# Performance work log

Measured on AMD Instinct MI355X. Metric: run time of the kernel, lower is better.

Reference implementation:

```python
import jax, jax.numpy as jnp
import numpy as np

N, E, D = 10000, 160000, 256
EPS = 1e-5


def layer_norm(x, gamma, beta):
    mu = jnp.mean(x, axis=-1, keepdims=True)
    var = jnp.var(x, axis=-1, keepdims=True)
    return (x - mu) * jax.lax.rsqrt(var + EPS) * gamma + beta


def mlp(x, w1, b1, w2, b2):
    return jax.nn.relu(x @ w1 + b1) @ w2 + b2


def setup_inputs() -> dict:
    key = jax.random.key(0)
    ks = jax.random.split(key, 16)
    s = lambda fan_in: 1.0 / np.sqrt(fan_in)
    inp = {
        'x': jax.random.normal(ks[0], (N, D), jnp.float32),
        'edge_index': jax.random.randint(ks[1], (2, E), 0, N, jnp.int64),
        'edge_attr': jax.random.normal(ks[2], (E, D), jnp.float32),
        # edge MLP: in 3D=768 -> hidden 2D=512 -> out D=256, then LN
        'e_w1': jax.random.uniform(ks[3], (3 * D, 2 * D), jnp.float32, -s(3 * D), s(3 * D)),
        'e_b1': jnp.zeros((2 * D,), jnp.float32),
        'e_w2': jax.random.uniform(ks[4], (2 * D, D), jnp.float32, -s(2 * D), s(2 * D)),
        'e_b2': jnp.zeros((D,), jnp.float32),
        'e_g': jnp.ones((D,), jnp.float32),
        'e_beta': jnp.zeros((D,), jnp.float32),
        # node MLP: in 2D=512 -> hidden 2D=512 -> out D=256, then LN
        'n_w1': jax.random.uniform(ks[5], (2 * D, 2 * D), jnp.float32, -s(2 * D), s(2 * D)),
        'n_b1': jnp.zeros((2 * D,), jnp.float32),
        'n_w2': jax.random.uniform(ks[6], (2 * D, D), jnp.float32, -s(2 * D), s(2 * D)),
        'n_b2': jnp.zeros((D,), jnp.float32),
        'n_g': jnp.ones((D,), jnp.float32),
        'n_beta': jnp.zeros((D,), jnp.float32),
    }
    return inp


def reference(x, edge_index, edge_attr, e_w1, e_b1, e_w2, e_b2, e_g, e_beta,
              n_w1, n_b1, n_w2, n_b2, n_g, n_beta):
    i, j = edge_index[0], edge_index[1]
    # Edge processor: gather, concat, MLP + LN, residual
    h = jnp.concatenate([x[i], x[j], edge_attr], axis=-1)  # [E, 3D]
    new_edge = edge_attr + layer_norm(mlp(h, e_w1, e_b1, e_w2, e_b2), e_g, e_beta)
    # Node processor: scatter-add over j, concat, MLP + LN, residual
    agg = jax.ops.segment_sum(new_edge, j, num_segments=x.shape[0])  # [N, D]
    hn = jnp.concatenate([x, agg], axis=-1)  # [N, 2D]
    new_x = x + layer_norm(mlp(hn, n_w1, n_b1, n_w2, n_b2), n_g, n_beta)
    return new_x, new_edge
```

## Files before the change

kernel.cpp:

```cpp
#include <hip/hip_runtime.h>

#define NNODE 10000
#define NEDGE 160000
#define DD 256

using f32x4  = __attribute__((ext_vector_type(4))) float;
using bf16x8 = __attribute__((ext_vector_type(8))) short;
using u32x4  = __attribute__((ext_vector_type(4))) unsigned;

__device__ inline short f2bf(float f) {
  unsigned u = __float_as_uint(f);
  unsigned r = (u + 0x7fffu + ((u >> 16) & 1u)) >> 16;
  return (short)(unsigned short)r;
}

__device__ inline float bf2f(short s) {
  return __uint_as_float(((unsigned)(unsigned short)s) << 16);
}

__device__ inline unsigned pkbf(float a, float b) {
  unsigned r;
  asm("v_cvt_pk_bf16_f32 %0, %1, %2" : "=v"(r) : "v"(a), "v"(b));
  return r;
}

__global__ void cast_x_kernel(const float* __restrict__ x, short* __restrict__ xb, int total) {
  int i = blockIdx.x * 256 + threadIdx.x;
  if (i < total) xb[i] = f2bf(x[i]);
}

__global__ void pack_w_kernel(const float* __restrict__ w, short* __restrict__ p, int K, int N) {
  int idx = blockIdx.x * 256 + threadIdx.x;
  if (idx >= K * N) return;
  int k = idx / N, n = idx - k * N;
  p[(size_t)(k >> 3) * N * 8 + (size_t)n * 8 + (k & 7)] = f2bf(w[idx]);
}

__global__ void pack_ew1_kernel(const float* __restrict__ w, short* __restrict__ w1ap,
                                short* __restrict__ w1bp, short* __restrict__ w1cp) {
  int idx = blockIdx.x * 256 + threadIdx.x;
  if (idx >= 768 * 512) return;
  int k = idx >> 9, n = idx & 511;
  short v = f2bf(w[idx]);
  int kk = k & 255;
  short* dst = (k < 256) ? w1ap : (k < 512) ? w1bp : w1cp;
  dst[(size_t)(kk >> 3) * 512 * 8 + (size_t)n * 8 + (kk & 7)] = v;
}

__global__ void hist_kernel(const int* __restrict__ ei, int* __restrict__ deg) {
  int e = blockIdx.x * 256 + threadIdx.x;
  if (e < NEDGE) {
    int j = ei[NEDGE + e]; j = min(max(j, 0), NNODE - 1);
    atomicAdd(&deg[j], 1);
  }
}

__global__ void scan_kernel(const int* __restrict__ deg, int* __restrict__ row_start) {
  __shared__ int part[256];
  int t = threadIdx.x;
  const int CH = 40;
  int base = t * CH;
  int s = 0;
  for (int i = 0; i < CH; i++) {
    int idx = base + i;
    s += (idx < NNODE) ? deg[idx] : 0;
  }
  part[t] = s;
  __syncthreads();
  for (int off = 1; off < 256; off <<= 1) {
    int v = (t >= off) ? part[t - off] : 0;
    __syncthreads();
    part[t] += v;
    __syncthreads();
  }
  int run = (t == 0) ? 0 : part[t - 1];
  for (int i = 0; i < CH; i++) {
    int idx = base + i;
    if (idx < NNODE) { row_start[idx] = run; run += deg[idx]; }
  }
  if (t == 255) row_start[NNODE] = part[255];
}

__global__ void scatter_kernel(const int* __restrict__ ei, const int* __restrict__ row_start,
                               int* __restrict__ cursor, int* __restrict__ csr) {
  int e = blockIdx.x * 256 + threadIdx.x;
  if (e < NEDGE) {
    int j = ei[NEDGE + e]; j = min(max(j, 0), NNODE - 1);
    int p = atomicAdd(&cursor[j], 1);
    csr[row_start[j] + p] = e;
  }
}

__global__ __launch_bounds__(256, 2)
void precomp_pab(const short* __restrict__ xb, const short* __restrict__ w1bp,
                 short* __restrict__ pab) {
  __shared__ __align__(16) short abuf[2048 * 8];

  const int tid  = threadIdx.x;
  const int lane = tid & 63;
  const int wid  = tid >> 6;
  const int lhi  = lane >> 4;
  const int llo  = lane & 15;
  const int swz  = llo & 7;
  const int m0   = blockIdx.x * 64;

  #pragma unroll
  for (int q = 0; q < 8; q++) {
    int S = wid * 512 + q * 64 + lane;
    int row = S >> 5;
    int segp = S & 31;
    int seg = segp ^ (row & 7);
    int rowg = min(m0 + row, NNODE - 1);
    __builtin_amdgcn_global_load_lds(
        (const int*)((const char*)xb + (size_t)rowg * 512 + seg * 16),
        (int*)(abuf + (size_t)(wid * 512 + q * 64) * 8), 16, 0, 0);
  }
  __syncthreads();

  f32x4 acc1[4][8] = {};
  const bf16x8* bp1 = (const bf16x8*)w1bp;
  #pragma unroll
  for (int kk = 0; kk < 256; kk += 32) {
    const int ks = kk >> 3;
    bf16x8 a[4];
    #pragma unroll
    for (int mf = 0; mf < 4; mf++)
      a[mf] = *(const bf16x8*)(abuf + ((mf * 16 + llo) * 32 + ((ks + lhi) ^ swz)) * 8);
    const bf16x8* bb = bp1 + (size_t)(ks + lhi) * 512 + wid * 128 + llo;
    #pragma unroll
    for (int nf = 0; nf < 8; nf++) {
      bf16x8 b = bb[nf * 16];
      #pragma unroll
      for (int mf = 0; mf < 4; mf++)
        acc1[mf][nf] = __builtin_amdgcn_mfma_f32_16x16x32_bf16(a[mf], b, acc1[mf][nf], 0, 0, 0);
    }
  }

  #pragma unroll
  for (int mf = 0; mf < 4; mf++) {
    #pragma unroll
    for (int r = 0; r < 4; r++) {
      int row = m0 + mf * 16 + lhi * 4 + r;
      if (row < NNODE) {
        u32x4 wv = { pkbf(acc1[mf][0][r], acc1[mf][1][r]),
                     pkbf(acc1[mf][2][r], acc1[mf][3][r]),
                     pkbf(acc1[mf][4][r], acc1[mf][5][r]),
                     pkbf(acc1[mf][6][r], acc1[mf][7][r]) };
        *(u32x4*)(pab + (size_t)row * 512 + llo * 32 + wid * 8) = wv;
      }
    }
  }
}

__global__ __launch_bounds__(256, 2)
void fused_edge(const int* __restrict__ ei,
                const int* __restrict__ csr,
                const float* __restrict__ ea,
                const short* __restrict__ xb,
                const short* __restrict__ pab,
                const short* __restrict__ w1ap,
                const short* __restrict__ w1cp,
                const float* __restrict__ b1,
                const short* __restrict__ w2p,
                const float* __restrict__ b2,
                const float* __restrict__ gam,
                const float* __restrict__ bet,
                float* __restrict__ out,
                float* __restrict__ aggf)
{
  __shared__ __align__(16) char smem[66560];
  __shared__ int eidx[64], idxi[64], idxj[64];
  __shared__ float pS[256], pQ[256];

  short* abufE = (short*)smem;
  short* hid   = (short*)smem;
  float* outt  = (float*)smem;

  const int tid  = threadIdx.x;
  const int lane = tid & 63;
  const int wid  = tid >> 6;
  const int lhi  = lane >> 4;
  const int llo  = lane & 15;
  const int swz  = llo & 7;
  const int m0   = blockIdx.x * 64;
  const int bcol2 = wid * 64 + llo;

  if (tid < 64) {
    int e = csr[m0 + tid];
    eidx[tid] = e;
    int a = ei[e];
    int b = ei[NEDGE + e];
    idxi[tid] = min(max(a, 0), NNODE - 1);
    idxj[tid] = min(max(b, 0), NNODE - 1);
  }
  __syncthreads();

  const short* pXi[4];
  #pragma unroll
  for (int mf = 0; mf < 4; mf++)
    pXi[mf] = xb + (size_t)idxi[mf * 16 + llo] * DD;

  #pragma unroll
  for (int q = 0; q < 8; q++) {
    int S = q * 256 + tid;
    int row = S >> 5;
    int segp = S & 31;
    int seg = segp ^ (row & 7);
    const f32x4* src = (const f32x4*)(ea + (size_t)eidx[row] * 256 + seg * 8);
    f32x4 u0 = __builtin_nontemporal_load(src);
    f32x4 u1 = __builtin_nontemporal_load(src + 1);
    u32x4 qv = { pkbf(u0.x, u0.y), pkbf(u0.z, u0.w), pkbf(u1.x, u1.y), pkbf(u1.z, u1.w) };
    *(u32x4*)(abufE + (size_t)S * 8) = qv;
  }
  __syncthreads();

  f32x4 acc1[4][8] = {};
  {
    const bf16x8* bpC = (const bf16x8*)w1cp;
    #pragma unroll
    for (int kk = 0; kk < 256; kk += 32) {
      const int ks = kk >> 3;
      bf16x8 a[4];
      #pragma unroll
      for (int mf = 0; mf < 4; mf++)
        a[mf] = *(const bf16x8*)(abufE + ((mf * 16 + llo) * 32 + ((ks + lhi) ^ swz)) * 8);
      const bf16x8* bb = bpC + (size_t)(ks + lhi) * 512 + wid * 128 + llo;
      #pragma unroll
      for (int nf = 0; nf < 8; nf++) {
        bf16x8 b = bb[nf * 16];
        #pragma unroll
        for (int mf = 0; mf < 4; mf++)
          acc1[mf][nf] = __builtin_amdgcn_mfma_f32_16x16x32_bf16(a[mf], b, acc1[mf][nf], 0, 0, 0);
      }
    }
    const bf16x8* bpA = (const bf16x8*)w1ap;
    #pragma unroll
    for (int kk = 0; kk < 256; kk += 32) {
      const int ks = kk >> 3;
      bf16x8 a[4];
      #pragma unroll
      for (int mf = 0; mf < 4; mf++)
        a[mf] = *(const bf16x8*)(pXi[mf] + kk + lhi * 8);
      const bf16x8* bb = bpA + (size_t)(ks + lhi) * 512 + wid * 128 + llo;
      #pragma unroll
      for (int nf = 0; nf < 8; nf++) {
        bf16x8 b = bb[nf * 16];
        #pragma unroll
        for (int mf = 0; mf < 4; mf++)
          acc1[mf][nf] = __builtin_amdgcn_mfma_f32_16x16x32_bf16(a[mf], b, acc1[mf][nf], 0, 0, 0);
      }
    }
  }

  #pragma unroll
  for (int mf = 0; mf < 4; mf++) {
    #pragma unroll
    for (int r = 0; r < 4; r++) {
      int row = mf * 16 + lhi * 4 + r;
      int gj = idxj[row];
      bf16x8 pb = *(const bf16x8*)(pab + (size_t)gj * 512 + llo * 32 + wid * 8);
      #pragma unroll
      for (int nf = 0; nf < 8; nf++)
        acc1[mf][nf][r] += bf2f(pb[nf]);
    }
  }

  float resv[4][4][4];
  #pragma unroll
  for (int mf = 0; mf < 4; mf++) {
    #pragma unroll
    for (int r = 0; r < 4; r++) {
      int row = mf * 16 + lhi * 4 + r;
      #pragma unroll
      for (int nf = 0; nf < 4; nf++) {
        int col = bcol2 + nf * 16;
        resv[mf][r][nf] = bf2f(abufE[row * 256 + (((col >> 3) ^ (row & 7)) << 3) + (col & 7)]);
      }
    }
  }
  __syncthreads();

  #pragma unroll
  for (int nf = 0; nf < 8; nf++) {
    int col = wid * 128 + nf * 16 + llo;
    float bb = b1[col];
    int cs = col >> 3, cl = col & 7;
    #pragma unroll
    for (int mf = 0; mf < 4; mf++) {
      #pragma unroll
      for (int r = 0; r < 4; r++) {
        int row = mf * 16 + lhi * 4 + r;
        float v = acc1[mf][nf][r] + bb;
        v = v > 0.f ? v : 0.f;
        hid[row * 512 + ((cs ^ (row & 7)) * 8) + cl] = f2bf(v);
      }
    }
  }
  __syncthreads();

  f32x4 acc2[4][4] = {};
  const bf16x8* bp2 = (const bf16x8*)w2p;
  #pragma unroll
  for (int kk = 0; kk < 512; kk += 32) {
    const int ks = kk >> 3;
    bf16x8 a[4];
    #pragma unroll
    for (int mf = 0; mf < 4; mf++) {
      int row = mf * 16 + llo;
      a[mf] = *(const bf16x8*)(hid + row * 512 + (((ks + lhi) ^ swz) * 8));
    }
    const bf16x8* bb = bp2 + (size_t)(ks + lhi) * 256 + bcol2;
    #pragma unroll
    for (int nf = 0; nf < 4; nf++) {
      bf16x8 b = bb[nf * 16];
      #pragma unroll
      for (int mf = 0; mf < 4; mf++)
        acc2[mf][nf] = __builtin_amdgcn_mfma_f32_16x16x32_bf16(a[mf], b, acc2[mf][nf], 0, 0, 0);
    }
  }

  float bb2[4], gg[4], be[4];
  #pragma unroll
  for (int nf = 0; nf < 4; nf++) {
    int col = bcol2 + nf * 16;
    bb2[nf] = b2[col]; gg[nf] = gam[col]; be[nf] = bet[col];
  }
  #pragma unroll
  for (int mf = 0; mf < 4; mf++)
    #pragma unroll
    for (int nf = 0; nf < 4; nf++)
      #pragma unroll
      for (int r = 0; r < 4; r++)
        acc2[mf][nf][r] += bb2[nf];

  float S[4][4], Q[4][4];
  #pragma unroll
  for (int mf = 0; mf < 4; mf++) {
    #pragma unroll
    for (int r = 0; r < 4; r++) {
      float s = 0.f, q = 0.f;
      #pragma unroll
      for (int nf = 0; nf < 4; nf++) {
        float v = acc2[mf][nf][r];
        s += v; q += v * v;
      }
      S[mf][r] = s; Q[mf][r] = q;
    }
  }
  #pragma unroll
  for (int m = 1; m <= 8; m <<= 1) {
    #pragma unroll
    for (int mf = 0; mf < 4; mf++)
      #pragma unroll
      for (int r = 0; r < 4; r++) {
        S[mf][r] += __shfl_xor(S[mf][r], m);
        Q[mf][r] += __shfl_xor(Q[mf][r], m);
      }
  }
  if (llo == 0) {
    #pragma unroll
    for (int mf = 0; mf < 4; mf++)
      #pragma unroll
      for (int r = 0; r < 4; r++) {
        int row = mf * 16 + lhi * 4 + r;
        pS[wid * 64 + row] = S[mf][r];
        pQ[wid * 64 + row] = Q[mf][r];
      }
  }
  __syncthreads();

  float mu[4][4], rsv[4][4];
  #pragma unroll
  for (int mf = 0; mf < 4; mf++) {
    #pragma unroll
    for (int r = 0; r < 4; r++) {
      int row = mf * 16 + lhi * 4 + r;
      float s = pS[row] + pS[64 + row] + pS[128 + row] + pS[192 + row];
      float q = pQ[row] + pQ[64 + row] + pQ[128 + row] + pQ[192 + row];
      float m_ = s * (1.f / 256.f);
      mu[mf][r]  = m_;
      rsv[mf][r] = rsqrtf(q * (1.f / 256.f) - m_ * m_ + 1e-5f);
    }
  }

  #pragma unroll
  for (int mf = 0; mf < 4; mf++) {
    #pragma unroll
    for (int r = 0; r < 4; r++) {
      int row = mf * 16 + lhi * 4 + r;
      #pragma unroll
      for (int nf = 0; nf < 4; nf++) {
        float v = (acc2[mf][nf][r] - mu[mf][r]) * rsv[mf][r] * gg[nf] + be[nf]
                  + resv[mf][r][nf];
        outt[row * 260 + bcol2 + nf * 16] = v;
      }
    }
  }
  __syncthreads();

  #pragma unroll
  for (int it = 0; it < 16; it++) {
    int row = it * 4 + wid;
    int e = eidx[row];
    f32x4 o4 = *((const f32x4*)(outt + row * 260) + lane);
    __builtin_nontemporal_store(o4, (f32x4*)(out + (size_t)e * 256) + lane);
  }
  __syncthreads();

  {
    int c = tid;
    float acc = 0.f;
    int cj = idxj[0];
    #pragma unroll 8
    for (int r = 0; r < 64; r++) {
      int jr = idxj[r];
      if (jr != cj) {
        atomicAdd(&aggf[(size_t)cj * 256 + c], acc);
        acc = 0.f; cj = jr;
      }
      acc += outt[r * 260 + c];
    }
    atomicAdd(&aggf[(size_t)cj * 256 + c], acc);
  }
}

__global__ __launch_bounds__(256, 2)
void fused_node(const float* __restrict__ x,
                const short* __restrict__ xb,
                const float* __restrict__ aggf,
                const short* __restrict__ w1p,
                const float* __restrict__ b1,
                const short* __restrict__ w2p,
                const float* __restrict__ b2,
                const float* __restrict__ gam,
                const float* __restrict__ bet,
                float* __restrict__ out)
{
  constexpr int HP = 520;
  __shared__ __align__(16) short hid[64 * HP];
  __shared__ float pS[4][64], pQ[4][64];

  const int tid  = threadIdx.x;
  const int lane = tid & 63;
  const int wid  = tid >> 6;
  const int m0   = blockIdx.x * 64;
  const int lhi  = lane >> 4;
  const int llo  = lane & 15;

  const short* pI[4]; const float* pJ[4];
  #pragma unroll
  for (int mf = 0; mf < 4; mf++) {
    int rr = min(m0 + mf * 16 + llo, NNODE - 1);
    pI[mf] = xb + (size_t)rr * DD;
    pJ[mf] = aggf + (size_t)rr * DD;
  }

  f32x4 acc1[4][8] = {};
  const bf16x8* bp1 = (const bf16x8*)w1p;
  const int bcol1 = wid * 128 + llo;

  #pragma unroll
  for (int s = 0; s < 8; s++) {
    #pragma unroll
    for (int kk = 0; kk < 64; kk += 32) {
      const int ko = s * 64 + kk + lhi * 8;
      bf16x8 a[4];
      #pragma unroll
      for (int mf = 0; mf < 4; mf++) {
        if (s < 4) {
          a[mf] = *(const bf16x8*)(pI[mf] + ko);
        } else {
          const float* fp = pJ[mf] + (ko - 256);
          f32x4 u0 = *(const f32x4*)fp;
          f32x4 u1 = *(const f32x4*)(fp + 4);
          u32x4 q = { pkbf(u0.x, u0.y), pkbf(u0.z, u0.w),
                      pkbf(u1.x, u1.y), pkbf(u1.z, u1.w) };
          a[mf] = __builtin_bit_cast(bf16x8, q);
        }
      }
      const bf16x8* bb = bp1 + (size_t)(s * 8 + (kk >> 3) + lhi) * 512 + bcol1;
      #pragma unroll
      for (int nf = 0; nf < 8; nf++) {
        bf16x8 b = bb[nf * 16];
        #pragma unroll
        for (int mf = 0; mf < 4; mf++)
          acc1[mf][nf] = __builtin_amdgcn_mfma_f32_16x16x32_bf16(a[mf], b, acc1[mf][nf], 0, 0, 0);
      }
    }
  }

  #pragma unroll
  for (int nf = 0; nf < 8; nf++) {
    int col = wid * 128 + nf * 16 + llo;
    float bb = b1[col];
    #pragma unroll
    for (int mf = 0; mf < 4; mf++) {
      #pragma unroll
      for (int r = 0; r < 4; r++) {
        float v = acc1[mf][nf][r] + bb;
        v = v > 0.f ? v : 0.f;
        hid[(mf * 16 + lhi * 4 + r) * HP + col] = f2bf(v);
      }
    }
  }
  __syncthreads();

  f32x4 acc2[4][4] = {};
  const bf16x8* bp2 = (const bf16x8*)w2p;
  const int bcol2 = wid * 64 + llo;
  #pragma unroll
  for (int kk = 0; kk < 512; kk += 32) {
    bf16x8 a[4];
    #pragma unroll
    for (int mf = 0; mf < 4; mf++)
      a[mf] = *(const bf16x8*)(hid + (mf * 16 + llo) * HP + kk + lhi * 8);
    const bf16x8* bb = bp2 + (size_t)((kk >> 3) + lhi) * 256 + bcol2;
    #pragma unroll
    for (int nf = 0; nf < 4; nf++) {
      bf16x8 b = bb[nf * 16];
      #pragma unroll
      for (int mf = 0; mf < 4; mf++)
        acc2[mf][nf] = __builtin_amdgcn_mfma_f32_16x16x32_bf16(a[mf], b, acc2[mf][nf], 0, 0, 0);
    }
  }

  float bb2[4], gg[4], be[4];
  #pragma unroll
  for (int nf = 0; nf < 4; nf++) {
    int col = bcol2 + nf * 16;
    bb2[nf] = b2[col]; gg[nf] = gam[col]; be[nf] = bet[col];
  }
  #pragma unroll
  for (int mf = 0; mf < 4; mf++)
    #pragma unroll
    for (int nf = 0; nf < 4; nf++)
      #pragma unroll
      for (int r = 0; r < 4; r++)
        acc2[mf][nf][r] += bb2[nf];

  float S[4][4], Q[4][4];
  #pragma unroll
  for (int mf = 0; mf < 4; mf++) {
    #pragma unroll
    for (int r = 0; r < 4; r++) {
      float s = 0.f, q = 0.f;
      #pragma unroll
      for (int nf = 0; nf < 4; nf++) {
        float v = acc2[mf][nf][r];
        s += v; q += v * v;
      }
      S[mf][r] = s; Q[mf][r] = q;
    }
  }
  #pragma unroll
  for (int m = 1; m <= 8; m <<= 1) {
    #pragma unroll
    for (int mf = 0; mf < 4; mf++)
      #pragma unroll
      for (int r = 0; r < 4; r++) {
        S[mf][r] += __shfl_xor(S[mf][r], m);
        Q[mf][r] += __shfl_xor(Q[mf][r], m);
      }
  }
  if (llo == 0) {
    #pragma unroll
    for (int mf = 0; mf < 4; mf++)
      #pragma unroll
      for (int r = 0; r < 4; r++) {
        int row = mf * 16 + lhi * 4 + r;
        pS[wid][row] = S[mf][r];
        pQ[wid][row] = Q[mf][r];
      }
  }
  __syncthreads();

  float mu[4][4], rsv[4][4];
  #pragma unroll
  for (int mf = 0; mf < 4; mf++) {
    #pragma unroll
    for (int r = 0; r < 4; r++) {
      int row = mf * 16 + lhi * 4 + r;
      float s = pS[0][row] + pS[1][row] + pS[2][row] + pS[3][row];
      float q = pQ[0][row] + pQ[1][row] + pQ[2][row] + pQ[3][row];
      float m_ = s * (1.f / 256.f);
      mu[mf][r]  = m_;
      rsv[mf][r] = rsqrtf(q * (1.f / 256.f) - m_ * m_ + 1e-5f);
    }
  }

  #pragma unroll
  for (int mf = 0; mf < 4; mf++) {
    #pragma unroll
    for (int r = 0; r < 4; r++) {
      int grow = m0 + mf * 16 + lhi * 4 + r;
      if (grow >= NNODE) continue;
      const float* rp = x   + (size_t)grow * DD + bcol2;
      float*       op = out + (size_t)grow * DD + bcol2;
      #pragma unroll
      for (int nf = 0; nf < 4; nf++) {
        float v = (acc2[mf][nf][r] - mu[mf][r]) * rsv[mf][r] * gg[nf] + be[nf] + rp[nf * 16];
        op[nf * 16] = v;
      }
    }
  }
}

extern "C" void kernel_launch(void* const* d_in, const int* in_sizes, int n_in,
                              void* d_out, int out_size, void* d_ws, size_t ws_size,
                              hipStream_t stream) {
  const float* x      = (const float*)d_in[0];
  const int*   ei     = (const int*)  d_in[1];
  const float* ea     = (const float*)d_in[2];
  const float* e_w1   = (const float*)d_in[3];
  const float* e_b1   = (const float*)d_in[4];
  const float* e_w2   = (const float*)d_in[5];
  const float* e_b2   = (const float*)d_in[6];
  const float* e_g    = (const float*)d_in[7];
  const float* e_beta = (const float*)d_in[8];
  const float* n_w1   = (const float*)d_in[9];
  const float* n_b1   = (const float*)d_in[10];
  const float* n_w2   = (const float*)d_in[11];
  const float* n_b2   = (const float*)d_in[12];
  const float* n_g    = (const float*)d_in[13];
  const float* n_beta = (const float*)d_in[14];

  float* out_x = (float*)d_out;
  float* out_e = (float*)d_out + (size_t)NNODE * DD;

  char* w = (char*)d_ws;
  short* xb    = (short*)(w);
  short* pab   = (short*)(w + 5120000);
  short* w1ap  = (short*)(w + 15360000);
  short* w1bp  = (short*)(w + 15622144);
  short* w1cp  = (short*)(w + 15884288);
  short* ew2p  = (short*)(w + 16146432);
  short* nw1p  = (short*)(w + 16408576);
  short* nw2p  = (short*)(w + 16932864);
  float* aggf  = (float*)(w + 17195008);
  int*   deg   = (int*)  (w + 27435008);
  int*   cur   = (int*)  (w + 27475968);
  int*   rs    = (int*)  (w + 27516928);
  int*   csr   = (int*)  (w + 27557904);

  hipMemsetAsync(deg, 0, 81920, stream);
  hipMemsetAsync(aggf, 0, (size_t)NNODE * DD * sizeof(float), stream);

  cast_x_kernel<<<(NNODE * DD + 255) / 256, 256, 0, stream>>>(x, xb, NNODE * DD);
  pack_ew1_kernel<<<(768 * 512 + 255) / 256, 256, 0, stream>>>(e_w1, w1ap, w1bp, w1cp);
  pack_w_kernel<<<(512 * 512 + 255) / 256, 256, 0, stream>>>(n_w1, nw1p, 512, 512);
  pack_w_kernel<<<(512 * 256 + 255) / 256, 256, 0, stream>>>(e_w2, ew2p, 512, 256);
  pack_w_kernel<<<(512 * 256 + 255) / 256, 256, 0, stream>>>(n_w2, nw2p, 512, 256);

  hist_kernel<<<(NEDGE + 255) / 256, 256, 0, stream>>>(ei, deg);
  scan_kernel<<<1, 256, 0, stream>>>(deg, rs);
  scatter_kernel<<<(NEDGE + 255) / 256, 256, 0, stream>>>(ei, rs, cur, csr);

  precomp_pab<<<(NNODE + 63) / 64, 256, 0, stream>>>(xb, w1bp, pab);

  fused_edge<<<NEDGE / 64, 256, 0, stream>>>(ei, csr, ea, xb, pab, w1ap, w1cp, e_b1,
                                             ew2p, e_b2, e_g, e_beta, out_e, aggf);
  fused_node<<<(NNODE + 63) / 64, 256, 0, stream>>>(x, xb, aggf, nw1p, n_b1,
                                                    nw2p, n_b2, n_g, n_beta, out_x);
}
```

Baseline: 527.7 us.

## Shrink edge kernel LDS by splitting hidden layer into halves for higher occupancy

Cuts the edge kernel's shared memory from about 65 KB to about 33 KB. The 512-wide hidden activation is now staged in two 256-column halves, with each half written by two waves and consumed by the second GEMM in turn. The residual is re-read from global fp32 edge_attr and outputs are written directly to global. The scatter-add buffer holds bf16 new_edge values rather than fp32. Launch bounds rise to 4 blocks per CU to raise occupancy, which risks register spills and adds extra syncs, strided global stores, and bf16 rounding in the aggregation.

Result: slower. 1.347 ms (+155.2%).

```diff
diff --git a/kernel.cpp b/kernel.cpp
--- a/kernel.cpp
+++ b/kernel.cpp
@@ -152,7 +152,7 @@
   }
 }
 
-__global__ __launch_bounds__(256, 2)
+__global__ __launch_bounds__(256, 4)
 void fused_edge(const int* __restrict__ ei,
                 const int* __restrict__ csr,
                 const float* __restrict__ ea,
@@ -168,13 +168,13 @@
                 float* __restrict__ out,
                 float* __restrict__ aggf)
 {
-  __shared__ __align__(16) char smem[66560];
+  __shared__ __align__(16) short R[64 * 264];
   __shared__ int eidx[64], idxi[64], idxj[64];
   __shared__ float pS[256], pQ[256];
 
-  short* abufE = (short*)smem;
-  short* hid   = (short*)smem;
-  float* outt  = (float*)smem;
+  short* abufE = R;
+  short* hid   = R;
+  short* nebuf = R;
 
   const int tid  = threadIdx.x;
   const int lane = tid & 63;
@@ -207,8 +207,8 @@
     int segp = S & 31;
     int seg = segp ^ (row & 7);
     const f32x4* src = (const f32x4*)(ea + (size_t)eidx[row] * 256 + seg * 8);
-    f32x4 u0 = __builtin_nontemporal_load(src);
-    f32x4 u1 = __builtin_nontemporal_load(src + 1);
+    f32x4 u0 = src[0];
+    f32x4 u1 = src[1];
     u32x4 qv = { pkbf(u0.x, u0.y), pkbf(u0.z, u0.w), pkbf(u1.x, u1.y), pkbf(u1.z, u1.w) };
     *(u32x4*)(abufE + (size_t)S * 8) = qv;
   }
@@ -264,59 +264,51 @@
         acc1[mf][nf][r] += bf2f(pb[nf]);
     }
   }
-
-  float resv[4][4][4];
-  #pragma unroll
-  for (int mf = 0; mf < 4; mf++) {
-    #pragma unroll
-    for (int r = 0; r < 4; r++) {
-      int row = mf * 16 + lhi * 4 + r;
-      #pragma unroll
-      for (int nf = 0; nf < 4; nf++) {
-        int col = bcol2 + nf * 16;
-        resv[mf][r][nf] = bf2f(abufE[row * 256 + (((col >> 3) ^ (row & 7)) << 3) + (col & 7)]);
-      }
-    }
-  }
-  __syncthreads();
-
-  #pragma unroll
-  for (int nf = 0; nf < 8; nf++) {
-    int col = wid * 128 + nf * 16 + llo;
-    float bb = b1[col];
-    int cs = col >> 3, cl = col & 7;
-    #pragma unroll
-    for (int mf = 0; mf < 4; mf++) {
-      #pragma unroll
-      for (int r = 0; r < 4; r++) {
-        int row = mf * 16 + lhi * 4 + r;
-        float v = acc1[mf][nf][r] + bb;
-        v = v > 0.f ? v : 0.f;
-        hid[row * 512 + ((cs ^ (row & 7)) * 8) + cl] = f2bf(v);
-      }
-    }
-  }
   __syncthreads();
 
   f32x4 acc2[4][4] = {};
   const bf16x8* bp2 = (const bf16x8*)w2p;
   #pragma unroll
-  for (int kk = 0; kk < 512; kk += 32) {
-    const int ks = kk >> 3;
-    bf16x8 a[4];
-    #pragma unroll
-    for (int mf = 0; mf < 4; mf++) {
-      int row = mf * 16 + llo;
-      a[mf] = *(const bf16x8*)(hid + row * 512 + (((ks + lhi) ^ swz) * 8));
-    }
-    const bf16x8* bb = bp2 + (size_t)(ks + lhi) * 256 + bcol2;
-    #pragma unroll
-    for (int nf = 0; nf < 4; nf++) {
-      bf16x8 b = bb[nf * 16];
-      #pragma unroll
-      for (int mf = 0; mf < 4; mf++)
-        acc2[mf][nf] = __builtin_amdgcn_mfma_f32_16x16x32_bf16(a[mf], b, acc2[mf][nf], 0, 0, 0);
-    }
+  for (int h = 0; h < 2; h++) {
+    if ((wid >> 1) == h) {
+      #pragma unroll
+      for (int nf = 0; nf < 8; nf++) {
+        int clocal = (wid & 1) * 128 + nf * 16 + llo;
+        float bb = b1[h * 256 + clocal];
+        int cs = clocal >> 3, cl = clocal & 7;
+        #pragma unroll
+        for (int mf = 0; mf < 4; mf++) {
+          #pragma unroll
+          for (int r = 0; r < 4; r++) {
+            int row = mf * 16 + lhi * 4 + r;
+            float v = acc1[mf][nf][r] + bb;
+            v = v > 0.f ? v : 0.f;
+            hid[row * 256 + ((cs ^ (row & 7)) << 3) + cl] = f2bf(v);
+          }
+        }
+      }
+    }
+    __syncthreads();
+
+    #pragma unroll
+    for (int kk = 0; kk < 256; kk += 32) {
+      const int ks = kk >> 3;
+      bf16x8 a[4];
+      #pragma unroll
+      for (int mf = 0; mf < 4; mf++) {
+        int row = mf * 16 + llo;
+        a[mf] = *(const bf16x8*)(hid + row * 256 + (((ks + lhi) ^ swz) << 3));
+      }
+      const bf16x8* bb = bp2 + (size_t)(h * 32 + ks + lhi) * 256 + bcol2;
+      #pragma unroll
+      for (int nf = 0; nf < 4; nf++) {
+        bf16x8 b = bb[nf * 16];
+        #pragma unroll
+        for (int mf = 0; mf < 4; mf++)
+          acc2[mf][nf] = __builtin_amdgcn_mfma_f32_16x16x32_bf16(a[mf], b, acc2[mf][nf], 0, 0, 0);
+      }
+    }
+    __syncthreads();
   }
 
   float bb2[4], gg[4], be[4];
@@ -369,7 +361,7 @@
   }
   __syncthreads();
 
-  float mu[4][4], rsv[4][4];
+  float mu[4][4], rstd[4][4];
   #pragma unroll
   for (int mf = 0; mf < 4; mf++) {
     #pragma unroll
@@ -378,8 +370,8 @@
       float s = pS[row] + pS[64 + row] + pS[128 + row] + pS[192 + row];
       float q = pQ[row] + pQ[64 + row] + pQ[128 + row] + pQ[192 + row];
       float m_ = s * (1.f / 256.f);
-      mu[mf][r]  = m_;
-      rsv[mf][r] = rsqrtf(q * (1.f / 256.f) - m_ * m_ + 1e-5f);
+      mu[mf][r]   = m_;
+      rstd[mf][r] = rsqrtf(q * (1.f / 256.f) - m_ * m_ + 1e-5f);
     }
   }
 
@@ -388,22 +380,17 @@
     #pragma unroll
     for (int r = 0; r < 4; r++) {
       int row = mf * 16 + lhi * 4 + r;
+      int e = eidx[row];
+      const float* rp = ea  + (size_t)e * DD + bcol2;
+      float*       op = out + (size_t)e * DD + bcol2;
       #pragma unroll
       for (int nf = 0; nf < 4; nf++) {
-        float v = (acc2[mf][nf][r] - mu[mf][r]) * rsv[mf][r] * gg[nf] + be[nf]
-                  + resv[mf][r][nf];
-        outt[row * 260 + bcol2 + nf * 16] = v;
-      }
-    }
-  }
-  __syncthreads();
-
-  #pragma unroll
-  for (int it = 0; it < 16; it++) {
-    int row = it * 4 + wid;
-    int e = eidx[row];
-    f32x4 o4 = *((const f32x4*)(outt + row * 260) + lane);
-    __builtin_nontemporal_store(o4, (f32x4*)(out + (size_t)e * 256) + lane);
+        float v = (acc2[mf][nf][r] - mu[mf][r]) * rstd[mf][r] * gg[nf] + be[nf]
+                  + rp[nf * 16];
+        op[nf * 16] = v;
+        nebuf[row * 264 + bcol2 + nf * 16] = f2bf(v);
+      }
+    }
   }
   __syncthreads();
 
@@ -418,7 +405,7 @@
         atomicAdd(&aggf[(size_t)cj * 256 + c], acc);
         acc = 0.f; cj = jr;
       }
-      acc += outt[r * 260 + c];
+      acc += bf2f(nebuf[r * 264 + c]);
     }
     atomicAdd(&aggf[(size_t)cj * 256 + c], acc);
   }
@@ -574,7 +561,7 @@
   }
   __syncthreads();
 
-  float mu[4][4], rsv[4][4];
+  float mu[4][4], rstd[4][4];
   #pragma unroll
   for (int mf = 0; mf < 4; mf++) {
     #pragma unroll
@@ -583,8 +570,8 @@
       float s = pS[0][row] + pS[1][row] + pS[2][row] + pS[3][row];
       float q = pQ[0][row] + pQ[1][row] + pQ[2][row] + pQ[3][row];
       float m_ = s * (1.f / 256.f);
-      mu[mf][r]  = m_;
-      rsv[mf][r] = rsqrtf(q * (1.f / 256.f) - m_ * m_ + 1e-5f);
+      mu[mf][r]   = m_;
+      rstd[mf][r] = rsqrtf(q * (1.f / 256.f) - m_ * m_ + 1e-5f);
     }
   }
 
@@ -598,7 +585,7 @@
       float*       op = out + (size_t)grow * DD + bcol2;
       #pragma unroll
       for (int nf = 0; nf < 4; nf++) {
-        float v = (acc2[mf][nf][r] - mu[mf][r]) * rsv[mf][r] * gg[nf] + be[nf] + rp[nf * 16];
+        float v = (acc2[mf][nf][r] - mu[mf][r]) * rstd[mf][r] * gg[nf] + be[nf] + rp[nf * 16];
         op[nf * 16] = v;
       }
     }
```
